# Optimization experiments

Hardware: AMD Instinct MI355X
Metric: run time of the kernel (lower is better)

The kernel has to match this reference:

```python
import jax, jax.numpy as jnp
import numpy as np

N = 100000   # nodes
E = 1600000  # edges (avg degree 16)
F_IN, H1, H2, H3, C = 500, 200, 100, 40, 3


def setup_inputs() -> dict:
    key = jax.random.key(0)
    ks = jax.random.split(key, 10)
    def w(k, shape, fan_in):
        return jax.random.normal(k, shape, dtype=jnp.float32) / np.sqrt(fan_in)
    return {
        "x": jax.random.normal(ks[0], (N, F_IN), dtype=jnp.float32),
        "edge_index": jax.random.randint(ks[1], (2, E), 0, N, dtype=jnp.int32),
        "W1": w(ks[2], (H1, F_IN), F_IN), "b1": jnp.zeros((H1,), jnp.float32),
        "W1b": w(ks[3], (H2, H1), H1),  "b1b": jnp.zeros((H2,), jnp.float32),
        "W2b": w(ks[4], (H3, H2), H2),  "b2b": jnp.zeros((H3,), jnp.float32),
        "W2": w(ks[5], (C, H3), H3),    "b2": jnp.zeros((C,), jnp.float32),
    }


def _gcn_conv(x, W, b, src, dst, norm_e, n):
    # GCNConv: linear transform, then normalized scatter-add aggregation, then bias
    h = x @ W.T                                   # [N, out]
    msgs = h[src] * norm_e[:, None]               # [E+N, out] gathered, normalized
    out = jax.ops.segment_sum(msgs, dst, num_segments=n)
    return out + b


def reference(x, edge_index, W1, b1, W1b, b1b, W2b, b2b, W2, b2):
    n = x.shape[0]
    loop = jnp.arange(n, dtype=edge_index.dtype)
    src = jnp.concatenate([edge_index[0], loop])  # add self-loops (GCNConv default)
    dst = jnp.concatenate([edge_index[1], loop])
    # symmetric normalization: deg computed on target nodes, norm = d^-1/2[src]*d^-1/2[dst]
    deg = jax.ops.segment_sum(jnp.ones_like(dst, dtype=x.dtype), dst, num_segments=n)
    dinv = jnp.where(deg > 0, jax.lax.rsqrt(deg), 0.0)
    norm_e = dinv[src] * dinv[dst]

    # dropout(p=0.5, training=self.training) is identity at inference
    h = jax.nn.relu(_gcn_conv(x, W1, b1, src, dst, norm_e, n))
    h = jax.nn.relu(_gcn_conv(h, W1b, b1b, src, dst, norm_e, n))
    h = jax.nn.relu(_gcn_conv(h, W2b, b2b, src, dst, norm_e, n))
    return _gcn_conv(h, W2, b2, src, dst, norm_e, n)
```

## Files before the change

### kernel.cpp

```cpp
#include <hip/hip_runtime.h>


#define DEV __device__ __forceinline__

typedef __attribute__((ext_vector_type(8))) short short8;
typedef __attribute__((ext_vector_type(4))) float f32x4;
typedef __attribute__((ext_vector_type(4))) _Float16 f16x4;

DEV unsigned short f2bf(float x) {
    unsigned u = __builtin_bit_cast(unsigned, x);
    u += 0x7FFFu + ((u >> 16) & 1u);
    return (unsigned short)(u >> 16);
}
DEV float bf2f(unsigned short b) {
    return __builtin_bit_cast(float, (unsigned)b << 16);
}

DEV void gload_lds16(const void* g, void* l) {
    __builtin_amdgcn_global_load_lds(
        (const __attribute__((address_space(1))) unsigned int*)g,
        (__attribute__((address_space(3))) unsigned int*)l, 16, 0, 0);
}


__global__ void k_init(int* __restrict__ cnt, int* __restrict__ fill, int n) {
    int i = blockIdx.x * 256 + threadIdx.x;
    if (i < n) { cnt[i] = 1; fill[i] = 0; }
}

__global__ void k_count(const int* __restrict__ dst, int* __restrict__ cnt, int E) {
    int e = blockIdx.x * 256 + threadIdx.x;
    if (e < E) atomicAdd(&cnt[dst[e]], 1);
}

__global__ void k_scan1(const int* __restrict__ cnt, int* __restrict__ row_start,
                        int* __restrict__ partial, float* __restrict__ dinv, int n) {
    __shared__ int sdata[256];
    int base = blockIdx.x * 1024;
    int t = threadIdx.x;
    int v[4]; int sum = 0;
#pragma unroll
    for (int j = 0; j < 4; ++j) {
        int idx = base + t * 4 + j;
        v[j] = (idx < n) ? cnt[idx] : 0;
        if (idx < n) dinv[idx] = rsqrtf((float)v[j]);
        sum += v[j];
    }
    sdata[t] = sum;
    __syncthreads();
    for (int off = 1; off < 256; off <<= 1) {
        int x = (t >= off) ? sdata[t - off] : 0;
        __syncthreads();
        sdata[t] += x;
        __syncthreads();
    }
    int excl = sdata[t] - sum;
#pragma unroll
    for (int j = 0; j < 4; ++j) {
        int idx = base + t * 4 + j;
        if (idx < n) row_start[idx] = excl;
        excl += v[j];
    }
    if (t == 255) partial[blockIdx.x] = sdata[255];
}

__global__ void k_scan2(int* __restrict__ partial, int nb) {
    __shared__ int s[128];
    int t = threadIdx.x;
    int v = (t < nb) ? partial[t] : 0;
    s[t] = v;
    __syncthreads();
    for (int off = 1; off < 128; off <<= 1) {
        int x = (t >= off) ? s[t - off] : 0;
        __syncthreads();
        s[t] += x;
        __syncthreads();
    }
    if (t < nb) partial[t] = s[t] - v;
}

__global__ void k_scan3(int* __restrict__ row_start, const int* __restrict__ partial,
                        int n, int total) {
    int i = blockIdx.x * 256 + threadIdx.x;
    if (i < n) row_start[i] += partial[i >> 10];
    if (i == 0) row_start[n] = total;
}

__global__ void k_fill(const int* __restrict__ src, const int* __restrict__ dst,
                       const int* __restrict__ row_start, int* __restrict__ fill,
                       int* __restrict__ csr_src, int E, int n) {
    int i = blockIdx.x * 256 + threadIdx.x;
    int total = E + n;
    if (i >= total) return;
    int s, d;
    if (i < E) { s = src[i]; d = dst[i]; }
    else       { s = d = i - E; }
    int pos = row_start[d] + atomicAdd(&fill[d], 1);
    csr_src[pos] = s;
}


__global__ void k_wdec(const float* __restrict__ W, int N, int K,
                       unsigned short* __restrict__ Wh, unsigned short* __restrict__ Wl,
                       int NPAD, int KPAD) {
    int i = blockIdx.x * 256 + threadIdx.x;
    if (i >= NPAD * KPAD) return;
    int r = i / KPAD, k = i - r * KPAD;
    float x = (r < N && k < K) ? W[r * K + k] : 0.f;
    unsigned short h = f2bf(x);
    unsigned short l = f2bf(x - bf2f(h));
    Wh[i] = h; Wl[i] = l;
}


struct A8 { f32x4 lo, hi; };

template <int NF, typename AT>
__global__ __launch_bounds__(512, 2)
void gemm_mfma(const AT* __restrict__ A, int lda, int M, int K,
               const unsigned short* __restrict__ Wh,
               const unsigned short* __restrict__ Wl, int ldw,
               const float* __restrict__ dinv,
               _Float16* __restrict__ H16, int ldh, int Nout) {
    constexpr int NPAD = NF * 16;
    constexpr int HBUF = NPAD * 64;
    constexpr int BUFB = 2 * HBUF;
    constexpr int CH   = NPAD * 4;
    constexpr int CH2  = 2 * CH;
    constexpr int NISS = CH2 / 64;
    __shared__ char lds[2 * BUFB];

    const int tid  = threadIdx.x;
    const int wv   = tid >> 6;
    const int lane = tid & 63;
    const int lr   = lane & 15;
    const int kq   = lane >> 4;
    const int m0   = blockIdx.x * 128;

    int arow = m0 + wv * 16 + lr;
    if (arow >= M) arow = M - 1;
    const AT* Arow = A + (size_t)arow * lda;

    auto stageW = [&](int s, int bufsel) {
        const int kb = s * 32;
        char* base = lds + bufsel * BUFB;
        for (int i = wv; i < NISS; i += 8) {
            int c  = i * 64 + lane;
            int h  = (c >= CH) ? 1 : 0;
            int cc = c - h * CH;
            int r  = cc >> 2;
            int sl = cc & 3;
            int gs = sl ^ (r & 3);
            const unsigned short* gp = (h ? Wl : Wh) + (size_t)r * ldw + kb + gs * 8;
            gload_lds16(gp, base + i * 1024);
        }
    };

    auto loadA = [&](int s) -> A8 {
        A8 o;
        int kb = s * 32 + kq * 8;
        if (kb + 8 <= K) {
            if constexpr (sizeof(AT) == 4) {
                const float* ap = (const float*)Arow + kb;
                o.lo = *(const f32x4*)ap;
                o.hi = *(const f32x4*)(ap + 4);
            } else {
                const _Float16* ap = (const _Float16*)Arow + kb;
                f16x4 v0 = *(const f16x4*)ap;
                f16x4 v1 = *(const f16x4*)(ap + 4);
                o.lo = __builtin_convertvector(v0, f32x4);
                o.hi = __builtin_convertvector(v1, f32x4);
            }
        } else {
#pragma unroll
            for (int i = 0; i < 4; ++i) {
                int k0 = kb + i, k1 = kb + 4 + i;
                o.lo[i] = (k0 < K) ? (float)Arow[k0] : 0.f;
                o.hi[i] = (k1 < K) ? (float)Arow[k1] : 0.f;
            }
        }
        return o;
    };

    f32x4 acc[NF];
#pragma unroll
    for (int f = 0; f < NF; ++f) acc[f] = (f32x4){0.f, 0.f, 0.f, 0.f};

    const int nsteps = (K + 31) / 32;

    stageW(0, 0);
    A8 acur = loadA(0);
    __syncthreads();

    const int ro = lr * 64 + ((kq ^ (lr & 3)) << 4);

    for (int s = 0; s < nsteps; ++s) {
        const char* bb = lds + (s & 1) * BUFB;
        const bool more = (s + 1 < nsteps);

        if (more) stageW(s + 1, (s + 1) & 1);
        A8 anxt;
        if (more) anxt = loadA(s + 1);
        else      { anxt.lo = (f32x4){0,0,0,0}; anxt.hi = (f32x4){0,0,0,0}; }

        float av[8];
#pragma unroll
        for (int i = 0; i < 4; ++i) { av[i] = acur.lo[i]; av[4 + i] = acur.hi[i]; }
        short8 ahi, alo;
#pragma unroll
        for (int i = 0; i < 8; ++i) {
            unsigned short h = f2bf(av[i]);
            ahi[i] = (short)h;
            alo[i] = (short)f2bf(av[i] - bf2f(h));
        }

#pragma unroll
        for (int f = 0; f < NF; ++f) {
            short8 bh = *(const short8*)(bb + f * 1024 + ro);
            short8 bl = *(const short8*)(bb + HBUF + f * 1024 + ro);
            acc[f] = __builtin_amdgcn_mfma_f32_16x16x32_bf16(ahi, bh, acc[f], 0, 0, 0);
            acc[f] = __builtin_amdgcn_mfma_f32_16x16x32_bf16(ahi, bl, acc[f], 0, 0, 0);
            acc[f] = __builtin_amdgcn_mfma_f32_16x16x32_bf16(alo, bh, acc[f], 0, 0, 0);
        }

        __syncthreads();
        acur = anxt;
    }

    const int rbase = m0 + wv * 16 + kq * 4;
    float dv[4];
#pragma unroll
    for (int j = 0; j < 4; ++j) {
        int row = rbase + j;
        dv[j] = (row < M) ? dinv[row] : 0.f;
    }
#pragma unroll
    for (int f = 0; f < NF; ++f) {
        int col = f * 16 + lr;
        if (col >= Nout) continue;
#pragma unroll
        for (int j = 0; j < 4; ++j) {
            int row = rbase + j;
            if (row < M) H16[(size_t)row * ldh + col] = (_Float16)(acc[f][j] * dv[j]);
        }
    }
}


template <int F, bool RELU>
__global__ __launch_bounds__(256)
void agg_f16(const _Float16* __restrict__ h, const int* __restrict__ row_start,
             const int* __restrict__ csr_src, const float* __restrict__ dinv,
             const float* __restrict__ bias, _Float16* __restrict__ out, int n) {
    constexpr int LPN = F / 4;
    constexpr int NPW = 64 / LPN;
    int wave = blockIdx.x * 4 + (threadIdx.x >> 6);
    int lane = threadIdx.x & 63;
    int sub  = lane / LPN;
    int fi   = lane - sub * LPN;
    int node = wave * NPW + sub;
    if (sub >= NPW || node >= n) return;
    int f = fi * 4;
    const _Float16* hf = h + f;

    f32x4 acc = {0.f, 0.f, 0.f, 0.f};
    int e0 = row_start[node], e1 = row_start[node + 1];
    int e = e0;
    for (; e + 4 <= e1; e += 4) {
        int s0 = csr_src[e + 0];
        int s1 = csr_src[e + 1];
        int s2 = csr_src[e + 2];
        int s3 = csr_src[e + 3];
        f16x4 v0 = *(const f16x4*)&hf[(size_t)s0 * F];
        f16x4 v1 = *(const f16x4*)&hf[(size_t)s1 * F];
        f16x4 v2 = *(const f16x4*)&hf[(size_t)s2 * F];
        f16x4 v3 = *(const f16x4*)&hf[(size_t)s3 * F];
        acc += __builtin_convertvector(v0, f32x4);
        acc += __builtin_convertvector(v1, f32x4);
        acc += __builtin_convertvector(v2, f32x4);
        acc += __builtin_convertvector(v3, f32x4);
    }
    for (; e < e1; ++e) {
        int s = csr_src[e];
        f16x4 v = *(const f16x4*)&hf[(size_t)s * F];
        acc += __builtin_convertvector(v, f32x4);
    }
    float dn = dinv[node];
    f32x4 b4 = *(const f32x4*)&bias[f];
    acc = acc * dn + b4;
    if (RELU) {
#pragma unroll
        for (int j = 0; j < 4; ++j) acc[j] = fmaxf(acc[j], 0.f);
    }
    f16x4 o;
#pragma unroll
    for (int j = 0; j < 4; ++j) o[j] = (_Float16)acc[j];
    *(f16x4*)&out[(size_t)node * F + f] = o;
}


__global__ void gemm_small(const _Float16* __restrict__ A, const float* __restrict__ B,
                           const float* __restrict__ dinv, float* __restrict__ C,
                           int M, int K) {
    int m = blockIdx.x * 256 + threadIdx.x;
    if (m >= M) return;
    float a0 = 0.f, a1 = 0.f, a2 = 0.f;
    for (int k = 0; k < K; ++k) {
        float a = (float)A[(size_t)m * K + k];
        a0 += a * B[0 * K + k];
        a1 += a * B[1 * K + k];
        a2 += a * B[2 * K + k];
    }
    float dv = dinv[m];
    C[(size_t)m * 3 + 0] = a0 * dv;
    C[(size_t)m * 3 + 1] = a1 * dv;
    C[(size_t)m * 3 + 2] = a2 * dv;
}

__global__ void agg_f3(const float* __restrict__ h, const int* __restrict__ row_start,
                       const int* __restrict__ csr_src, const float* __restrict__ dinv,
                       const float* __restrict__ bias, float* __restrict__ out, int n) {
    int i = blockIdx.x * 256 + threadIdx.x;
    if (i >= n * 3) return;
    int node = i / 3;
    int f = i - node * 3;
    float acc = 0.f;
    int e1 = row_start[node + 1];
    for (int e = row_start[node]; e < e1; ++e) {
        int s = csr_src[e];
        acc += h[(size_t)s * 3 + f];
    }
    out[i] = acc * dinv[node] + bias[f];
}


extern "C" void kernel_launch(void* const* d_in, const int* in_sizes, int n_in,
                              void* d_out, int out_size, void* d_ws, size_t ws_size,
                              hipStream_t stream) {
    const float* x   = (const float*)d_in[0];
    const int*   ei  = (const int*)d_in[1];
    const float* W1  = (const float*)d_in[2];
    const float* b1  = (const float*)d_in[3];
    const float* W1b = (const float*)d_in[4];
    const float* b1b = (const float*)d_in[5];
    const float* W2b = (const float*)d_in[6];
    const float* b2b = (const float*)d_in[7];
    const float* W2  = (const float*)d_in[8];
    const float* b2  = (const float*)d_in[9];
    float* out = (float*)d_out;

    const int F_IN = 500, H1 = 200, H2 = 100, H3 = 40;
    const int N = in_sizes[0] / F_IN;
    const int E = in_sizes[1] / 2;
    const int* src = ei;
    const int* dst = ei + E;

    size_t off = 0;
    auto alloc = [&](size_t bytes) -> void* {
        void* p = (char*)d_ws + off;
        off += (bytes + 255) & ~(size_t)255;
        return p;
    };
    int*   cnt       = (int*)  alloc((size_t)N * 4);
    int*   row_start = (int*)  alloc((size_t)(N + 1) * 4);
    int*   fill      = (int*)  alloc((size_t)N * 4);
    int*   partial   = (int*)  alloc(128 * 4);
    float* dinv      = (float*)alloc((size_t)N * 4);
    int*   csr_src   = (int*)  alloc((size_t)(E + N) * 4);
    unsigned short* wh1 = (unsigned short*)alloc(208 * 512 * 2);
    unsigned short* wl1 = (unsigned short*)alloc(208 * 512 * 2);
    unsigned short* wh2 = (unsigned short*)alloc(112 * 224 * 2);
    unsigned short* wl2 = (unsigned short*)alloc(112 * 224 * 2);
    unsigned short* wh3 = (unsigned short*)alloc(48 * 128 * 2);
    unsigned short* wl3 = (unsigned short*)alloc(48 * 128 * 2);
    _Float16* h16   = (_Float16*)alloc((size_t)N * H1 * 2);
    _Float16* act16 = (_Float16*)alloc((size_t)N * H1 * 2);
    float*    bufC  = (float*)   alloc((size_t)N * 3 * 4);

    int gN  = (N + 255) / 256;
    int gE  = (E + 255) / 256;
    int gEN = (E + N + 255) / 256;
    int nb  = (N + 1023) / 1024;

    k_init <<<gN, 256, 0, stream>>>(cnt, fill, N);
    k_count<<<gE, 256, 0, stream>>>(dst, cnt, E);
    k_scan1<<<nb, 256, 0, stream>>>(cnt, row_start, partial, dinv, N);
    k_scan2<<<1, 128, 0, stream>>>(partial, nb);
    k_scan3<<<gN, 256, 0, stream>>>(row_start, partial, N, E + N);
    k_fill <<<gEN, 256, 0, stream>>>(src, dst, row_start, fill, csr_src, E, N);

    k_wdec<<<(208 * 512 + 255) / 256, 256, 0, stream>>>(W1,  H1, F_IN, wh1, wl1, 208, 512);
    k_wdec<<<(112 * 224 + 255) / 256, 256, 0, stream>>>(W1b, H2, H1,   wh2, wl2, 112, 224);
    k_wdec<<<( 48 * 128 + 255) / 256, 256, 0, stream>>>(W2b, H3, H2,   wh3, wl3,  48, 128);

    const int gG = (N + 127) / 128;

    gemm_mfma<13, float><<<gG, 512, 0, stream>>>(x, F_IN, N, F_IN, wh1, wl1, 512,
                                                 dinv, h16, H1, H1);
    agg_f16<200, true><<<(N + 3) / 4, 256, 0, stream>>>(h16, row_start, csr_src, dinv,
                                                        b1, act16, N);
    gemm_mfma<7, _Float16><<<gG, 512, 0, stream>>>(act16, H1, N, H1, wh2, wl2, 224,
                                                   dinv, h16, H2, H2);
    agg_f16<100, true><<<(N / 2 + 3) / 4, 256, 0, stream>>>(h16, row_start, csr_src, dinv,
                                                            b1b, act16, N);
    gemm_mfma<3, _Float16><<<gG, 512, 0, stream>>>(act16, H2, N, H2, wh3, wl3, 128,
                                                   dinv, h16, H3, H3);
    {
        int waves = (N + 5) / 6, blocks = (waves + 3) / 4;
        agg_f16<40, true><<<blocks, 256, 0, stream>>>(h16, row_start, csr_src, dinv,
                                                      b2b, act16, N);
    }
    gemm_small<<<(N + 255) / 256, 256, 0, stream>>>(act16, W2, dinv, bufC, N, H3);
    agg_f3<<<(N * 3 + 255) / 256, 256, 0, stream>>>(bufC, row_start, csr_src, dinv,
                                                    b2, out, N);
}
```

Before: 576.8 us.

## Use f16 MFMA with split weights for hidden GEMMs and 32-row waves

The hidden-layer GEMMs, whose activations are already f16, now feed f16 MFMA directly and split only the weights into f16 hi plus a scaled lo part. This drops the per-step bf16 hi/lo split of A and cuts the MFMA count from three per tile to two. Each wave now computes two 16-row tiles with 256-thread blocks, so every LDS weight fragment is reused across twice as many rows. The layer-2 activation gets a padded row stride of 112 so A loads can be 16-byte vectors. The cost is higher register pressure from the doubled accumulators, and the f16 weight split has a narrower exponent range than bf16.

New measurement: 577.3 us. Within noise of the previous version (+0.1%).

```diff
diff --git a/kernel.cpp b/kernel.cpp
--- a/kernel.cpp
+++ b/kernel.cpp
@@ -4,6 +4,7 @@
 #define DEV __device__ __forceinline__
 
 typedef __attribute__((ext_vector_type(8))) short short8;
+typedef __attribute__((ext_vector_type(8))) _Float16 f16x8;
 typedef __attribute__((ext_vector_type(4))) float f32x4;
 typedef __attribute__((ext_vector_type(4))) _Float16 f16x4;
 
@@ -99,7 +100,6 @@
     csr_src[pos] = s;
 }
 
-
 __global__ void k_wdec(const float* __restrict__ W, int N, int K,
                        unsigned short* __restrict__ Wh, unsigned short* __restrict__ Wl,
                        int NPAD, int KPAD) {
@@ -111,12 +111,24 @@
     unsigned short l = f2bf(x - bf2f(h));
     Wh[i] = h; Wl[i] = l;
 }
+__global__ void k_wdec16(const float* __restrict__ W, int N, int K,
+                         unsigned short* __restrict__ Wh, unsigned short* __restrict__ Wl,
+                         int NPAD, int KPAD) {
+    int i = blockIdx.x * 256 + threadIdx.x;
+    if (i >= NPAD * KPAD) return;
+    int r = i / KPAD, k = i - r * KPAD;
+    float x = (r < N && k < K) ? W[r * K + k] : 0.f;
+    _Float16 h = (_Float16)x;
+    _Float16 l = (_Float16)((x - (float)h) * 2048.0f);
+    Wh[i] = __builtin_bit_cast(unsigned short, h);
+    Wl[i] = __builtin_bit_cast(unsigned short, l);
+}
 
 
 struct A8 { f32x4 lo, hi; };
 
-template <int NF, typename AT>
-__global__ __launch_bounds__(512, 2)
+template <int NF, int MODE, typename AT>
+__global__ __launch_bounds__(256, 2)
 void gemm_mfma(const AT* __restrict__ A, int lda, int M, int K,
                const unsigned short* __restrict__ Wh,
                const unsigned short* __restrict__ Wl, int ldw,
@@ -137,14 +149,15 @@
     const int kq   = lane >> 4;
     const int m0   = blockIdx.x * 128;
 
-    int arow = m0 + wv * 16 + lr;
-    if (arow >= M) arow = M - 1;
-    const AT* Arow = A + (size_t)arow * lda;
+    int arow0 = m0 + wv * 32 + lr;       if (arow0 >= M) arow0 = M - 1;
+    int arow1 = m0 + wv * 32 + 16 + lr;  if (arow1 >= M) arow1 = M - 1;
+    const AT* Arow0 = A + (size_t)arow0 * lda;
+    const AT* Arow1 = A + (size_t)arow1 * lda;
 
     auto stageW = [&](int s, int bufsel) {
         const int kb = s * 32;
         char* base = lds + bufsel * BUFB;
-        for (int i = wv; i < NISS; i += 8) {
+        for (int i = wv; i < NISS; i += 4) {
             int c  = i * 64 + lane;
             int h  = (c >= CH) ? 1 : 0;
             int cc = c - h * CH;
@@ -156,21 +169,13 @@
         }
     };
 
-    auto loadA = [&](int s) -> A8 {
+    auto loadA32 = [&](const AT* Arow, int s) -> A8 {
         A8 o;
         int kb = s * 32 + kq * 8;
         if (kb + 8 <= K) {
-            if constexpr (sizeof(AT) == 4) {
-                const float* ap = (const float*)Arow + kb;
-                o.lo = *(const f32x4*)ap;
-                o.hi = *(const f32x4*)(ap + 4);
-            } else {
-                const _Float16* ap = (const _Float16*)Arow + kb;
-                f16x4 v0 = *(const f16x4*)ap;
-                f16x4 v1 = *(const f16x4*)(ap + 4);
-                o.lo = __builtin_convertvector(v0, f32x4);
-                o.hi = __builtin_convertvector(v1, f32x4);
-            }
+            const float* ap = (const float*)Arow + kb;
+            o.lo = *(const f32x4*)ap;
+            o.hi = *(const f32x4*)(ap + 4);
         } else {
 #pragma unroll
             for (int i = 0; i < 4; ++i) {
@@ -181,15 +186,31 @@
         }
         return o;
     };
-
-    f32x4 acc[NF];
-#pragma unroll
-    for (int f = 0; f < NF; ++f) acc[f] = (f32x4){0.f, 0.f, 0.f, 0.f};
-
-    const int nsteps = (K + 31) / 32;
+    auto loadA16 = [&](const AT* Arow, int s) -> short8 {
+        int kb = s * 32 + kq * 8;
+        if (kb + 8 <= K) return *(const short8*)((const unsigned short*)Arow + kb);
+        short8 o;
+        const unsigned short* ap = (const unsigned short*)Arow;
+#pragma unroll
+        for (int i = 0; i < 8; ++i) o[i] = (kb + i < K) ? (short)ap[kb + i] : (short)0;
+        return o;
+    };
+
+    f32x4 acP[NF], acQ[NF], alP[NF], alQ[NF];
+#pragma unroll
+    for (int f = 0; f < NF; ++f) {
+        acP[f] = (f32x4){0.f, 0.f, 0.f, 0.f};
+        acQ[f] = (f32x4){0.f, 0.f, 0.f, 0.f};
+        alP[f] = (f32x4){0.f, 0.f, 0.f, 0.f};
+        alQ[f] = (f32x4){0.f, 0.f, 0.f, 0.f};
+    }
+
+    const int nsteps = ldw / 32;
 
     stageW(0, 0);
-    A8 acur = loadA(0);
+    A8 a0c{}, a1c{}; short8 h0c{}, h1c{};
+    if constexpr (MODE == 0) { a0c = loadA32(Arow0, 0); a1c = loadA32(Arow1, 0); }
+    else                     { h0c = loadA16(Arow0, 0); h1c = loadA16(Arow1, 0); }
     __syncthreads();
 
     const int ro = lr * 64 + ((kq ^ (lr & 3)) << 4);
@@ -199,49 +220,99 @@
         const bool more = (s + 1 < nsteps);
 
         if (more) stageW(s + 1, (s + 1) & 1);
-        A8 anxt;
-        if (more) anxt = loadA(s + 1);
-        else      { anxt.lo = (f32x4){0,0,0,0}; anxt.hi = (f32x4){0,0,0,0}; }
-
-        float av[8];
-#pragma unroll
-        for (int i = 0; i < 4; ++i) { av[i] = acur.lo[i]; av[4 + i] = acur.hi[i]; }
-        short8 ahi, alo;
-#pragma unroll
-        for (int i = 0; i < 8; ++i) {
-            unsigned short h = f2bf(av[i]);
-            ahi[i] = (short)h;
-            alo[i] = (short)f2bf(av[i] - bf2f(h));
-        }
-
-#pragma unroll
-        for (int f = 0; f < NF; ++f) {
-            short8 bh = *(const short8*)(bb + f * 1024 + ro);
-            short8 bl = *(const short8*)(bb + HBUF + f * 1024 + ro);
-            acc[f] = __builtin_amdgcn_mfma_f32_16x16x32_bf16(ahi, bh, acc[f], 0, 0, 0);
-            acc[f] = __builtin_amdgcn_mfma_f32_16x16x32_bf16(ahi, bl, acc[f], 0, 0, 0);
-            acc[f] = __builtin_amdgcn_mfma_f32_16x16x32_bf16(alo, bh, acc[f], 0, 0, 0);
+        A8 a0n{}, a1n{}; short8 h0n{}, h1n{};
+        if (more) {
+            if constexpr (MODE == 0) { a0n = loadA32(Arow0, s + 1); a1n = loadA32(Arow1, s + 1); }
+            else                     { h0n = loadA16(Arow0, s + 1); h1n = loadA16(Arow1, s + 1); }
+        }
+
+        if constexpr (MODE == 0) {
+            float av0[8], av1[8];
+#pragma unroll
+            for (int i = 0; i < 4; ++i) {
+                av0[i] = a0c.lo[i]; av0[4 + i] = a0c.hi[i];
+                av1[i] = a1c.lo[i]; av1[4 + i] = a1c.hi[i];
+            }
+            short8 a0hi, a0lo, a1hi, a1lo;
+#pragma unroll
+            for (int i = 0; i < 8; ++i) {
+                unsigned short h0 = f2bf(av0[i]);
+                a0hi[i] = (short)h0; a0lo[i] = (short)f2bf(av0[i] - bf2f(h0));
+                unsigned short h1 = f2bf(av1[i]);
+                a1hi[i] = (short)h1; a1lo[i] = (short)f2bf(av1[i] - bf2f(h1));
+            }
+#pragma unroll
+            for (int f = 0; f < NF; ++f) {
+                short8 bh = *(const short8*)(bb + f * 1024 + ro);
+                short8 bl = *(const short8*)(bb + HBUF + f * 1024 + ro);
+                acP[f] = __builtin_amdgcn_mfma_f32_16x16x32_bf16(a0hi, bh, acP[f], 0, 0, 0);
+                acP[f] = __builtin_amdgcn_mfma_f32_16x16x32_bf16(a0hi, bl, acP[f], 0, 0, 0);
+                acP[f] = __builtin_amdgcn_mfma_f32_16x16x32_bf16(a0lo, bh, acP[f], 0, 0, 0);
+                acQ[f] = __builtin_amdgcn_mfma_f32_16x16x32_bf16(a1hi, bh, acQ[f], 0, 0, 0);
+                acQ[f] = __builtin_amdgcn_mfma_f32_16x16x32_bf16(a1hi, bl, acQ[f], 0, 0, 0);
+                acQ[f] = __builtin_amdgcn_mfma_f32_16x16x32_bf16(a1lo, bh, acQ[f], 0, 0, 0);
+            }
+        } else {
+            f16x8 a0 = __builtin_bit_cast(f16x8, h0c);
+            f16x8 a1 = __builtin_bit_cast(f16x8, h1c);
+#pragma unroll
+            for (int f = 0; f < NF; ++f) {
+                f16x8 bh = __builtin_bit_cast(f16x8, *(const short8*)(bb + f * 1024 + ro));
+                f16x8 bl = __builtin_bit_cast(f16x8, *(const short8*)(bb + HBUF + f * 1024 + ro));
+                acP[f] = __builtin_amdgcn_mfma_f32_16x16x32_f16(a0, bh, acP[f], 0, 0, 0);
+                alP[f] = __builtin_amdgcn_mfma_f32_16x16x32_f16(a0, bl, alP[f], 0, 0, 0);
+                acQ[f] = __builtin_amdgcn_mfma_f32_16x16x32_f16(a1, bh, acQ[f], 0, 0, 0);
+                alQ[f] = __builtin_amdgcn_mfma_f32_16x16x32_f16(a1, bl, alQ[f], 0, 0, 0);
+            }
         }
 
         __syncthreads();
-        acur = anxt;
-    }
-
-    const int rbase = m0 + wv * 16 + kq * 4;
-    float dv[4];
-#pragma unroll
-    for (int j = 0; j < 4; ++j) {
-        int row = rbase + j;
-        dv[j] = (row < M) ? dinv[row] : 0.f;
-    }
-#pragma unroll
-    for (int f = 0; f < NF; ++f) {
-        int col = f * 16 + lr;
-        if (col >= Nout) continue;
+        if constexpr (MODE == 0) { a0c = a0n; a1c = a1n; }
+        else                     { h0c = h0n; h1c = h1n; }
+    }
+
+    {
+        const int rbase = m0 + wv * 32 + kq * 4;
+        float dv[4];
 #pragma unroll
         for (int j = 0; j < 4; ++j) {
             int row = rbase + j;
-            if (row < M) H16[(size_t)row * ldh + col] = (_Float16)(acc[f][j] * dv[j]);
+            dv[j] = (row < M) ? dinv[row] : 0.f;
+        }
+#pragma unroll
+        for (int f = 0; f < NF; ++f) {
+            int col = f * 16 + lr;
+            if (col >= Nout) continue;
+#pragma unroll
+            for (int j = 0; j < 4; ++j) {
+                int row = rbase + j;
+                if (row >= M) continue;
+                float v = acP[f][j];
+                if constexpr (MODE == 1) v += alP[f][j] * (1.0f / 2048.0f);
+                H16[(size_t)row * ldh + col] = (_Float16)(v * dv[j]);
+            }
+        }
+    }
+    {
+        const int rbase = m0 + wv * 32 + 16 + kq * 4;
+        float dv[4];
+#pragma unroll
+        for (int j = 0; j < 4; ++j) {
+            int row = rbase + j;
+            dv[j] = (row < M) ? dinv[row] : 0.f;
+        }
+#pragma unroll
+        for (int f = 0; f < NF; ++f) {
+            int col = f * 16 + lr;
+            if (col >= Nout) continue;
+#pragma unroll
+            for (int j = 0; j < 4; ++j) {
+                int row = rbase + j;
+                if (row >= M) continue;
+                float v = acQ[f][j];
+                if constexpr (MODE == 1) v += alQ[f][j] * (1.0f / 2048.0f);
+                H16[(size_t)row * ldh + col] = (_Float16)(v * dv[j]);
+            }
         }
     }
 }
@@ -251,7 +322,8 @@
 __global__ __launch_bounds__(256)
 void agg_f16(const _Float16* __restrict__ h, const int* __restrict__ row_start,
              const int* __restrict__ csr_src, const float* __restrict__ dinv,
-             const float* __restrict__ bias, _Float16* __restrict__ out, int n) {
+             const float* __restrict__ bias, _Float16* __restrict__ out, int n,
+             int ldo) {
     constexpr int LPN = F / 4;
     constexpr int NPW = 64 / LPN;
     int wave = blockIdx.x * 4 + (threadIdx.x >> 6);
@@ -295,7 +367,7 @@
     f16x4 o;
 #pragma unroll
     for (int j = 0; j < 4; ++j) o[j] = (_Float16)acc[j];
-    *(f16x4*)&out[(size_t)node * F + f] = o;
+    *(f16x4*)&out[(size_t)node * ldo + f] = o;
 }
 
 
@@ -389,26 +461,26 @@
     k_scan3<<<gN, 256, 0, stream>>>(row_start, partial, N, E + N);
     k_fill <<<gEN, 256, 0, stream>>>(src, dst, row_start, fill, csr_src, E, N);
 
-    k_wdec<<<(208 * 512 + 255) / 256, 256, 0, stream>>>(W1,  H1, F_IN, wh1, wl1, 208, 512);
-    k_wdec<<<(112 * 224 + 255) / 256, 256, 0, stream>>>(W1b, H2, H1,   wh2, wl2, 112, 224);
-    k_wdec<<<( 48 * 128 + 255) / 256, 256, 0, stream>>>(W2b, H3, H2,   wh3, wl3,  48, 128);
+    k_wdec  <<<(208 * 512 + 255) / 256, 256, 0, stream>>>(W1,  H1, F_IN, wh1, wl1, 208, 512);
+    k_wdec16<<<(112 * 224 + 255) / 256, 256, 0, stream>>>(W1b, H2, H1,   wh2, wl2, 112, 224);
+    k_wdec16<<<( 48 * 128 + 255) / 256, 256, 0, stream>>>(W2b, H3, H2,   wh3, wl3,  48, 128);
 
     const int gG = (N + 127) / 128;
 
-    gemm_mfma<13, float><<<gG, 512, 0, stream>>>(x, F_IN, N, F_IN, wh1, wl1, 512,
-                                                 dinv, h16, H1, H1);
+    gemm_mfma<13, 0, float><<<gG, 256, 0, stream>>>(x, F_IN, N, F_IN, wh1, wl1, 512,
+                                                    dinv, h16, H1, H1);
     agg_f16<200, true><<<(N + 3) / 4, 256, 0, stream>>>(h16, row_start, csr_src, dinv,
-                                                        b1, act16, N);
-    gemm_mfma<7, _Float16><<<gG, 512, 0, stream>>>(act16, H1, N, H1, wh2, wl2, 224,
-                                                   dinv, h16, H2, H2);
+                                                        b1, act16, N, 200);
+    gemm_mfma<7, 1, _Float16><<<gG, 256, 0, stream>>>(act16, 200, N, H1, wh2, wl2, 224,
+                                                      dinv, h16, H2, H2);
     agg_f16<100, true><<<(N / 2 + 3) / 4, 256, 0, stream>>>(h16, row_start, csr_src, dinv,
-                                                            b1b, act16, N);
-    gemm_mfma<3, _Float16><<<gG, 512, 0, stream>>>(act16, H2, N, H2, wh3, wl3, 128,
-                                                   dinv, h16, H3, H3);
+                                                            b1b, act16, N, 112);
+    gemm_mfma<3, 1, _Float16><<<gG, 256, 0, stream>>>(act16, 112, N, H2, wh3, wl3, 128,
+                                                      dinv, h16, H3, H3);
     {
         int waves = (N + 5) / 6, blocks = (waves + 3) / 4;
         agg_f16<40, true><<<blocks, 256, 0, stream>>>(h16, row_start, csr_src, dinv,
-                                                      b2b, act16, N);
+                                                      b2b, act16, N, 40);
     }
     gemm_small<<<(N + 255) / 256, 256, 0, stream>>>(act16, W2, dinv, bufC, N, H3);
     agg_f3<<<(N * 3 + 255) / 256, 256, 0, stream>>>(bufC, row_start, csr_src, dinv,
```
